# Kernel optimization log

Measured on AMD Instinct MI355X. Metric: run time of the kernel, lower is better.

The kernel has to match this reference:

```python
import jax, jax.numpy as jnp
import numpy as np

B, T, IN = 32, 1024, 256
H = 128          # hidden_size
NL = 2           # num_layers
NC = 4           # num_classes
F2 = 2 * H       # bidirectional feature size


def _lstm_dir(xs, w_ih, w_hh, b_ih, b_hh, reverse):
    # xs: [T, B, in]; w_ih: [4H, in]; w_hh: [4H, H]
    if reverse:
        xs = xs[::-1]
    h0 = jnp.zeros((xs.shape[1], H), xs.dtype)
    c0 = jnp.zeros((xs.shape[1], H), xs.dtype)

    def step(carry, xt):
        h, c = carry
        g = xt @ w_ih.T + b_ih + h @ w_hh.T + b_hh  # [B, 4H]
        i, f, gg, o = jnp.split(g, 4, axis=-1)       # PyTorch gate order i,f,g,o
        c = jax.nn.sigmoid(f) * c + jax.nn.sigmoid(i) * jnp.tanh(gg)
        h = jax.nn.sigmoid(o) * jnp.tanh(c)
        return (h, c), h

    _, hs = jax.lax.scan(step, (h0, c0), xs)  # [T, B, H]
    if reverse:
        hs = hs[::-1]
    return hs


def setup_inputs() -> dict:
    key = jax.random.key(0)
    ks = jax.random.split(key, 12)
    s = 0.05
    x = jax.random.normal(ks[0], (B, T, IN), jnp.float32)
    # stacked LSTM params: [layer, direction, ...]; layer0 in = IN, layer1 in = 2H = IN
    w_ih = jax.random.normal(ks[1], (NL, 2, 4 * H, IN), jnp.float32) * s
    w_hh = jax.random.normal(ks[2], (NL, 2, 4 * H, H), jnp.float32) * s
    b_ih = jax.random.normal(ks[3], (NL, 2, 4 * H), jnp.float32) * s
    b_hh = jax.random.normal(ks[4], (NL, 2, 4 * H), jnp.float32) * s
    wq = jax.random.normal(ks[5], (F2, F2), jnp.float32) * s
    wk = jax.random.normal(ks[6], (F2, F2), jnp.float32) * s
    wv = jax.random.normal(ks[7], (F2, F2), jnp.float32) * s
    bq = jax.random.normal(ks[8], (F2,), jnp.float32) * s
    bk = jax.random.normal(ks[9], (F2,), jnp.float32) * s
    bv = jax.random.normal(ks[10], (F2,), jnp.float32) * s
    w_fc = jax.random.normal(ks[11], (NC, F2), jnp.float32) * s
    b_fc = jnp.zeros((NC,), jnp.float32)
    return {"x": x, "w_ih": w_ih, "w_hh": w_hh, "b_ih": b_ih, "b_hh": b_hh,
            "wq": wq, "wk": wk, "wv": wv, "bq": bq, "bk": bk, "bv": bv,
            "w_fc": w_fc, "b_fc": b_fc}


def reference(x, w_ih, w_hh, b_ih, b_hh, wq, wk, wv, bq, bk, bv, w_fc, b_fc):
    # --- biLSTM (eval mode: inter-layer dropout inactive) ---
    xs = jnp.swapaxes(x, 0, 1)  # time-major [T, B, IN]
    for l in range(NL):
        fwd = _lstm_dir(xs, w_ih[l, 0], w_hh[l, 0], b_ih[l, 0], b_hh[l, 0], False)
        bwd = _lstm_dir(xs, w_ih[l, 1], w_hh[l, 1], b_ih[l, 1], b_hh[l, 1], True)
        xs = jnp.concatenate([fwd, bwd], axis=-1)  # [T, B, 2H]
    out = jnp.swapaxes(xs, 0, 1)  # [B, T, 2H]
    # --- naive full self-attention ---
    q = out @ wq.T + bq
    k = out @ wk.T + bk
    v = out @ wv.T + bv
    scores = jnp.einsum('btd,bsd->bts', q, k) / jnp.sqrt(jnp.float32(F2))
    attn = jax.nn.softmax(scores, axis=-1)          # [B, T, T]
    ctx = jnp.einsum('bts,bsd->btd', attn, v)       # [B, T, 2H]
    # --- FC head on last timestep ---
    return ctx[:, -1, :] @ w_fc.T + b_fc            # [B, NC]
```

## Files before the change

### kernel.cpp

```cpp
#include <hip/hip_runtime.h>
#include <math.h>
#include <stdint.h>

#define BB 32
#define TT 1024
#define INF 256
#define HH 128
#define G4 512
#define CH 16

typedef _Float16 half2_t __attribute__((ext_vector_type(2)));
typedef __attribute__((address_space(3))) uint32_t lds_u32;
typedef __attribute__((address_space(1))) const uint32_t glb_u32;

__device__ __forceinline__ float fdot2f(half2_t a, half2_t b, float c) {
    return __builtin_amdgcn_fdot2(a, b, c, false);
}
__device__ __forceinline__ float rcpf(float x) {
    return __builtin_amdgcn_rcpf(x);
}
__device__ __forceinline__ float dpp_xor1(float x) {
    return __builtin_bit_cast(float, __builtin_amdgcn_update_dpp(
        0, __builtin_bit_cast(int, x), 0xB1, 0xF, 0xF, true));
}
__device__ __forceinline__ float dpp_xor2(float x) {
    return __builtin_bit_cast(float, __builtin_amdgcn_update_dpp(
        0, __builtin_bit_cast(int, x), 0x4E, 0xF, 0xF, true));
}
__device__ __forceinline__ void bar_lgkm() {
    asm volatile("s_waitcnt lgkmcnt(0)\n\ts_barrier" ::: "memory");
}

__global__ __launch_bounds__(256, 2) void gemm_inproj(
    const float* __restrict__ A,
    const float* __restrict__ w_ih_l,
    const float* __restrict__ b_ih_l,
    const float* __restrict__ b_hh_l,
    float* __restrict__ xproj)
{
    const int d  = blockIdx.z;
    const float* W = w_ih_l + (size_t)d * G4 * INF;
    float* C = xproj + (size_t)d * 32768 * 512;
    const int m0 = blockIdx.y * 128;
    const int n0 = blockIdx.x * 128;
    const int tid = threadIdx.x;
    const int tx = tid & 15, ty = tid >> 4;

    __shared__ __align__(16) half2_t As2[16 * 128];
    __shared__ __align__(16) half2_t Bs2[16 * 128];

    float acc[8][8] = {};
    const int lr = tid >> 1;
    const int lk = (tid & 1) * 16;

    float4 ar4[4], br4[4];
#pragma unroll
    for (int i = 0; i < 4; ++i) {
        ar4[i] = *(const float4*)(A + (size_t)(m0 + lr) * 256 + lk + 4 * i);
        br4[i] = *(const float4*)(W + (size_t)(n0 + lr) * 256 + lk + 4 * i);
    }

    for (int k0 = 0; k0 < 256; k0 += 32) {
        __syncthreads();
#pragma unroll
        for (int i = 0; i < 4; ++i) {
            const int kp = (lk >> 1) + 2 * i;
            As2[(kp + 0) * 128 + lr] = half2_t{(_Float16)ar4[i].x, (_Float16)ar4[i].y};
            As2[(kp + 1) * 128 + lr] = half2_t{(_Float16)ar4[i].z, (_Float16)ar4[i].w};
            Bs2[(kp + 0) * 128 + lr] = half2_t{(_Float16)br4[i].x, (_Float16)br4[i].y};
            Bs2[(kp + 1) * 128 + lr] = half2_t{(_Float16)br4[i].z, (_Float16)br4[i].w};
        }
        __syncthreads();
        if (k0 + 32 < 256) {
#pragma unroll
            for (int i = 0; i < 4; ++i) {
                ar4[i] = *(const float4*)(A + (size_t)(m0 + lr) * 256 + k0 + 32 + lk + 4 * i);
                br4[i] = *(const float4*)(W + (size_t)(n0 + lr) * 256 + k0 + 32 + lk + 4 * i);
            }
        }
#pragma unroll
        for (int kp = 0; kp < 16; ++kp) {
            half2_t av[8], bv[8];
            *(float4*)&av[0] = *(const float4*)&As2[kp * 128 + ty * 4];
            *(float4*)&av[4] = *(const float4*)&As2[kp * 128 + 64 + ty * 4];
            *(float4*)&bv[0] = *(const float4*)&Bs2[kp * 128 + tx * 4];
            *(float4*)&bv[4] = *(const float4*)&Bs2[kp * 128 + 64 + tx * 4];
#pragma unroll
            for (int i = 0; i < 8; ++i)
#pragma unroll
                for (int j = 0; j < 8; ++j)
                    acc[i][j] = fdot2f(av[i], bv[j], acc[i][j]);
        }
    }

    float bias[8];
#pragma unroll
    for (int j = 0; j < 8; ++j) {
        const int n = n0 + (j < 4 ? tx * 4 + j : 64 + tx * 4 + (j - 4));
        bias[j] = b_ih_l[d * G4 + n] + b_hh_l[d * G4 + n];
    }
#pragma unroll
    for (int i = 0; i < 8; ++i) {
        const int m = m0 + (i < 4 ? ty * 4 + i : 64 + ty * 4 + (i - 4));
        float4 o0, o1;
        o0.x = acc[i][0] + bias[0]; o0.y = acc[i][1] + bias[1];
        o0.z = acc[i][2] + bias[2]; o0.w = acc[i][3] + bias[3];
        o1.x = acc[i][4] + bias[4]; o1.y = acc[i][5] + bias[5];
        o1.z = acc[i][6] + bias[6]; o1.w = acc[i][7] + bias[7];
        *(float4*)(C + (size_t)m * 512 + n0 + tx * 4)      = o0;
        *(float4*)(C + (size_t)m * 512 + n0 + 64 + tx * 4) = o1;
    }
}

__global__ __launch_bounds__(512, 1) void lstm_rec(
    const float* __restrict__ xproj,
    const float* __restrict__ w_hh_l,
    float* __restrict__ out)
{
    const int b = blockIdx.x & 31;
    const int d = blockIdx.x >> 5;
    const int tid = threadIdx.x;
    const int wvid = tid >> 6;
    const int l = tid & 63;
    const int s = l & 3;
    const int g = l >> 2;
    const int j = (wvid << 4) | g;

    __shared__ __align__(16) _Float16 hs[HH];
    __shared__ __align__(16) float xbuf[2][CH * 512];
    __shared__ __align__(16) float obuf[CH * HH];

    half2_t wv[4][16];
#pragma unroll
    for (int G = 0; G < 4; ++G) {
        const float* wr = w_hh_l + (size_t)(d * G4 + 128 * G + j) * HH + 32 * s;
#pragma unroll
        for (int q4 = 0; q4 < 8; ++q4) {
            float4 f = *(const float4*)(wr + 4 * q4);
            wv[G][2 * q4]     = half2_t{(_Float16)f.x, (_Float16)f.y};
            wv[G][2 * q4 + 1] = half2_t{(_Float16)f.z, (_Float16)f.w};
        }
    }

    if (tid < 64) ((half2_t*)hs)[tid] = half2_t{(_Float16)0.f, (_Float16)0.f};
    float c = 0.f;

    const float* xp = xproj + ((size_t)d * BB + b) * TT * 512;
    float* ob = out + (size_t)b * TT * 256 + d * HH;

    {
        const int tlo = d ? 1008 : 0;
        const float* gsrc = xp + (size_t)tlo * 512;
#pragma unroll
        for (int i = 0; i < 4; ++i)
            __builtin_amdgcn_global_load_lds((glb_u32*)(gsrc + tid * 4 + i * 2048),
                                             (lds_u32*)&xbuf[0][tid * 4 + i * 2048],
                                             16, 0, 0);
    }
    __syncthreads();

    for (int ck = 0; ck < 64; ++ck) {
        const int cur = ck & 1;
        if (ck + 1 < 64) {
            const int tlo = d ? (1008 - (ck + 1) * CH) : (ck + 1) * CH;
            const float* gsrc = xp + (size_t)tlo * 512;
#pragma unroll
            for (int i = 0; i < 4; ++i)
                __builtin_amdgcn_global_load_lds((glb_u32*)(gsrc + tid * 4 + i * 2048),
                                                 (lds_u32*)&xbuf[cur ^ 1][tid * 4 + i * 2048],
                                                 16, 0, 0);
        }
        const float* xb = xbuf[cur];

#pragma unroll 1
        for (int si = 0; si < CH; ++si) {
            const int lds_t = d ? (CH - 1 - si) : si;

            const float xi = xb[lds_t * 512 +       j];
            const float xf = xb[lds_t * 512 + 128 + j];
            const float xg = xb[lds_t * 512 + 256 + j];
            const float xo = xb[lds_t * 512 + 384 + j];

            const float4* hp = (const float4*)(hs + 32 * s);
            float4 hA = hp[0], hB = hp[1], hC = hp[2], hD = hp[3];
            half2_t hh[16];
            hh[0]  = __builtin_bit_cast(half2_t, hA.x);
            hh[1]  = __builtin_bit_cast(half2_t, hA.y);
            hh[2]  = __builtin_bit_cast(half2_t, hA.z);
            hh[3]  = __builtin_bit_cast(half2_t, hA.w);
            hh[4]  = __builtin_bit_cast(half2_t, hB.x);
            hh[5]  = __builtin_bit_cast(half2_t, hB.y);
            hh[6]  = __builtin_bit_cast(half2_t, hB.z);
            hh[7]  = __builtin_bit_cast(half2_t, hB.w);
            hh[8]  = __builtin_bit_cast(half2_t, hC.x);
            hh[9]  = __builtin_bit_cast(half2_t, hC.y);
            hh[10] = __builtin_bit_cast(half2_t, hC.z);
            hh[11] = __builtin_bit_cast(half2_t, hC.w);
            hh[12] = __builtin_bit_cast(half2_t, hD.x);
            hh[13] = __builtin_bit_cast(half2_t, hD.y);
            hh[14] = __builtin_bit_cast(half2_t, hD.z);
            hh[15] = __builtin_bit_cast(half2_t, hD.w);

            float a0 = 0.f, a1 = 0.f, a2 = 0.f, a3 = 0.f;
            float e0 = 0.f, e1 = 0.f, e2 = 0.f, e3 = 0.f;
#pragma unroll
            for (int kk = 0; kk < 8; ++kk) {
                a0 = fdot2f(wv[0][kk], hh[kk], a0);
                a1 = fdot2f(wv[1][kk], hh[kk], a1);
                a2 = fdot2f(wv[2][kk], hh[kk], a2);
                a3 = fdot2f(wv[3][kk], hh[kk], a3);
                e0 = fdot2f(wv[0][kk + 8], hh[kk + 8], e0);
                e1 = fdot2f(wv[1][kk + 8], hh[kk + 8], e1);
                e2 = fdot2f(wv[2][kk + 8], hh[kk + 8], e2);
                e3 = fdot2f(wv[3][kk + 8], hh[kk + 8], e3);
            }
            a0 += e0; a1 += e1; a2 += e2; a3 += e3;

            a0 += dpp_xor1(a0); a0 += dpp_xor2(a0);
            a1 += dpp_xor1(a1); a1 += dpp_xor2(a1);
            a2 += dpp_xor1(a2); a2 += dpp_xor2(a2);
            a3 += dpp_xor1(a3); a3 += dpp_xor2(a3);

            const float gi = rcpf(1.f + __expf(-(a0 + xi)));
            const float gf = rcpf(1.f + __expf(-(a1 + xf)));
            const float gg = 1.f - 2.f * rcpf(1.f + __expf(2.f * (a2 + xg)));
            const float go = rcpf(1.f + __expf(-(a3 + xo)));
            c = gf * c + gi * gg;
            const float th = 1.f - 2.f * rcpf(1.f + __expf(2.f * c));
            const float h = go * th;
            if (s == 0) {
                hs[j] = (_Float16)h;
                obuf[si * HH + j] = h;
            }
            bar_lgkm();
        }

        {
            const int idx = tid * 4;
            const int sf = idx >> 7, jf = idx & 127;
            const int sg = ck * CH + sf;
            const int t  = d ? (TT - 1 - sg) : sg;
            float4 o0 = *(const float4*)&obuf[idx];
            *(float4*)&ob[(size_t)t * 256 + jf] = o0;
        }
        __syncthreads();
    }
}

__global__ __launch_bounds__(256) void attn_kernel(
    const float* __restrict__ out1,
    const float* __restrict__ wq, const float* __restrict__ bq,
    const float* __restrict__ wk,
    const float* __restrict__ wv, const float* __restrict__ bv,
    const float* __restrict__ wfc, const float* __restrict__ bfc,
    float* __restrict__ outp)
{
    const int b = blockIdx.x;
    const int tid = threadIdx.x;
    __shared__ float xl[256], q[256], u[256], cx[256];
    __shared__ __align__(16) float r[256];
    __shared__ float sc[TT];
    __shared__ float red[256];

    const float* ob = out1 + (size_t)b * TT * 256;

    xl[tid] = ob[(size_t)(TT - 1) * 256 + tid];
    __syncthreads();

    float acc = bq[tid];
    const float* wqr = wq + (size_t)tid * 256;
#pragma unroll 4
    for (int k = 0; k < 256; ++k) acc += xl[k] * wqr[k];
    q[tid] = acc;
    __syncthreads();

    acc = 0.f;
#pragma unroll 4
    for (int dd = 0; dd < 256; ++dd) acc += q[dd] * wk[(size_t)dd * 256 + tid];
    r[tid] = acc;
    __syncthreads();

    const int wave = tid >> 6, lane = tid & 63;
    float4 r4 = *(const float4*)&r[lane * 4];
    for (int t = wave; t < TT; t += 4) {
        float4 o4 = *(const float4*)(ob + (size_t)t * 256 + lane * 4);
        float p = r4.x * o4.x + r4.y * o4.y + r4.z * o4.z + r4.w * o4.w;
#pragma unroll
        for (int off = 32; off > 0; off >>= 1) p += __shfl_down(p, off, 64);
        if (lane == 0) sc[t] = p * 0.0625f;
    }
    __syncthreads();

    float mx = -1e30f;
#pragma unroll
    for (int i = 0; i < 4; ++i) mx = fmaxf(mx, sc[tid + 256 * i]);
    red[tid] = mx; __syncthreads();
    for (int st = 128; st > 0; st >>= 1) {
        if (tid < st) red[tid] = fmaxf(red[tid], red[tid + st]);
        __syncthreads();
    }
    mx = red[0]; __syncthreads();
    float lsum = 0.f;
#pragma unroll
    for (int i = 0; i < 4; ++i) {
        float e = expf(sc[tid + 256 * i] - mx);
        sc[tid + 256 * i] = e;
        lsum += e;
    }
    __syncthreads();
    red[tid] = lsum; __syncthreads();
    for (int st = 128; st > 0; st >>= 1) {
        if (tid < st) red[tid] += red[tid + st];
        __syncthreads();
    }
    const float inv = 1.f / red[0];
    __syncthreads();

    acc = 0.f;
#pragma unroll 8
    for (int t = 0; t < TT; ++t) acc += sc[t] * ob[(size_t)t * 256 + tid];
    u[tid] = acc * inv;
    __syncthreads();

    acc = bv[tid];
#pragma unroll 4
    for (int k = 0; k < 256; ++k) acc += u[k] * wv[(size_t)tid * 256 + k];
    cx[tid] = acc;
    __syncthreads();

    if (tid < 4) {
        float o = bfc[tid];
        for (int k = 0; k < 256; ++k) o += cx[k] * wfc[tid * 256 + k];
        outp[b * 4 + tid] = o;
    }
}

extern "C" void kernel_launch(void* const* d_in, const int* in_sizes, int n_in,
                              void* d_out, int out_size, void* d_ws, size_t ws_size,
                              hipStream_t stream)
{
    const float* x    = (const float*)d_in[0];
    const float* w_ih = (const float*)d_in[1];
    const float* w_hh = (const float*)d_in[2];
    const float* b_ih = (const float*)d_in[3];
    const float* b_hh = (const float*)d_in[4];
    const float* wq   = (const float*)d_in[5];
    const float* wk   = (const float*)d_in[6];
    const float* wv   = (const float*)d_in[7];
    const float* bq   = (const float*)d_in[8];
    const float* bv   = (const float*)d_in[10];
    const float* wfc  = (const float*)d_in[11];
    const float* bfcv = (const float*)d_in[12];
    float* outp = (float*)d_out;

    float* ws    = (float*)d_ws;
    float* xproj = ws;
    float* out0  = ws + 33554432;
    float* out1  = out0 + 8388608;

    dim3 gg(4, 256, 2);

    gemm_inproj<<<gg, 256, 0, stream>>>(x, w_ih, b_ih, b_hh, xproj);
    lstm_rec<<<64, 512, 0, stream>>>(xproj, w_hh, out0);
    gemm_inproj<<<gg, 256, 0, stream>>>(out0, w_ih + 2 * 512 * 256, b_ih + 1024, b_hh + 1024, xproj);
    lstm_rec<<<64, 512, 0, stream>>>(xproj, w_hh + 2 * 512 * 128, out1);
    attn_kernel<<<32, 256, 0, stream>>>(out1, wq, bq, wk, wv, bv, wfc, bfcv, outp);
}
```

Measured before the change: 1.786 ms.

## Fuse input projection GEMM into LSTM recurrence kernel with chunk-ahead pipelining

Removes the separate input-projection GEMM and its large xproj buffer. Each LSTM block now computes the projection for the next time chunk itself, interleaved with the current chunk's serial recurrent steps, and reads fp16 W_ih converted once by a small kernel. This saves a large global write and read and two kernel launches. In exchange, the latency-bound recurrent loop gains extra per-step dot-product work and global weight loads, and only 64 blocks do the projection, so it may slow the serial critical path.

```diff
diff --git a/kernel.cpp b/kernel.cpp
--- a/kernel.cpp
+++ b/kernel.cpp
@@ -4,14 +4,11 @@
 
 #define BB 32
 #define TT 1024
-#define INF 256
 #define HH 128
 #define G4 512
 #define CH 16
 
 typedef _Float16 half2_t __attribute__((ext_vector_type(2)));
-typedef __attribute__((address_space(3))) uint32_t lds_u32;
-typedef __attribute__((address_space(1))) const uint32_t glb_u32;
 
 __device__ __forceinline__ float fdot2f(half2_t a, half2_t b, float c) {
     return __builtin_amdgcn_fdot2(a, b, c, false);
@@ -31,89 +28,21 @@
     asm volatile("s_waitcnt lgkmcnt(0)\n\ts_barrier" ::: "memory");
 }
 
-__global__ __launch_bounds__(256, 2) void gemm_inproj(
-    const float* __restrict__ A,
-    const float* __restrict__ w_ih_l,
+__global__ __launch_bounds__(256) void cvt_wih(
+    const float* __restrict__ w, _Float16* __restrict__ o)
+{
+    const int i = (blockIdx.x * 256 + threadIdx.x) * 4;
+    float4 f = *(const float4*)(w + i);
+    half2_t t[2] = { half2_t{(_Float16)f.x, (_Float16)f.y},
+                     half2_t{(_Float16)f.z, (_Float16)f.w} };
+    *(float2*)(o + i) = *(float2*)t;
+}
+
+__global__ __launch_bounds__(512, 1) void lstm_fused(
+    const float* __restrict__ x_in,
+    const _Float16* __restrict__ wih16_l,
     const float* __restrict__ b_ih_l,
     const float* __restrict__ b_hh_l,
-    float* __restrict__ xproj)
-{
-    const int d  = blockIdx.z;
-    const float* W = w_ih_l + (size_t)d * G4 * INF;
-    float* C = xproj + (size_t)d * 32768 * 512;
-    const int m0 = blockIdx.y * 128;
-    const int n0 = blockIdx.x * 128;
-    const int tid = threadIdx.x;
-    const int tx = tid & 15, ty = tid >> 4;
-
-    __shared__ __align__(16) half2_t As2[16 * 128];
-    __shared__ __align__(16) half2_t Bs2[16 * 128];
-
-    float acc[8][8] = {};
-    const int lr = tid >> 1;
-    const int lk = (tid & 1) * 16;
-
-    float4 ar4[4], br4[4];
-#pragma unroll
-    for (int i = 0; i < 4; ++i) {
-        ar4[i] = *(const float4*)(A + (size_t)(m0 + lr) * 256 + lk + 4 * i);
-        br4[i] = *(const float4*)(W + (size_t)(n0 + lr) * 256 + lk + 4 * i);
-    }
-
-    for (int k0 = 0; k0 < 256; k0 += 32) {
-        __syncthreads();
-#pragma unroll
-        for (int i = 0; i < 4; ++i) {
-            const int kp = (lk >> 1) + 2 * i;
-            As2[(kp + 0) * 128 + lr] = half2_t{(_Float16)ar4[i].x, (_Float16)ar4[i].y};
-            As2[(kp + 1) * 128 + lr] = half2_t{(_Float16)ar4[i].z, (_Float16)ar4[i].w};
-            Bs2[(kp + 0) * 128 + lr] = half2_t{(_Float16)br4[i].x, (_Float16)br4[i].y};
-            Bs2[(kp + 1) * 128 + lr] = half2_t{(_Float16)br4[i].z, (_Float16)br4[i].w};
-        }
-        __syncthreads();
-        if (k0 + 32 < 256) {
-#pragma unroll
-            for (int i = 0; i < 4; ++i) {
-                ar4[i] = *(const float4*)(A + (size_t)(m0 + lr) * 256 + k0 + 32 + lk + 4 * i);
-                br4[i] = *(const float4*)(W + (size_t)(n0 + lr) * 256 + k0 + 32 + lk + 4 * i);
-            }
-        }
-#pragma unroll
-        for (int kp = 0; kp < 16; ++kp) {
-            half2_t av[8], bv[8];
-            *(float4*)&av[0] = *(const float4*)&As2[kp * 128 + ty * 4];
-            *(float4*)&av[4] = *(const float4*)&As2[kp * 128 + 64 + ty * 4];
-            *(float4*)&bv[0] = *(const float4*)&Bs2[kp * 128 + tx * 4];
-            *(float4*)&bv[4] = *(const float4*)&Bs2[kp * 128 + 64 + tx * 4];
-#pragma unroll
-            for (int i = 0; i < 8; ++i)
-#pragma unroll
-                for (int j = 0; j < 8; ++j)
-                    acc[i][j] = fdot2f(av[i], bv[j], acc[i][j]);
-        }
-    }
-
-    float bias[8];
-#pragma unroll
-    for (int j = 0; j < 8; ++j) {
-        const int n = n0 + (j < 4 ? tx * 4 + j : 64 + tx * 4 + (j - 4));
-        bias[j] = b_ih_l[d * G4 + n] + b_hh_l[d * G4 + n];
-    }
-#pragma unroll
-    for (int i = 0; i < 8; ++i) {
-        const int m = m0 + (i < 4 ? ty * 4 + i : 64 + ty * 4 + (i - 4));
-        float4 o0, o1;
-        o0.x = acc[i][0] + bias[0]; o0.y = acc[i][1] + bias[1];
-        o0.z = acc[i][2] + bias[2]; o0.w = acc[i][3] + bias[3];
-        o1.x = acc[i][4] + bias[4]; o1.y = acc[i][5] + bias[5];
-        o1.z = acc[i][6] + bias[6]; o1.w = acc[i][7] + bias[7];
-        *(float4*)(C + (size_t)m * 512 + n0 + tx * 4)      = o0;
-        *(float4*)(C + (size_t)m * 512 + n0 + 64 + tx * 4) = o1;
-    }
-}
-
-__global__ __launch_bounds__(512, 1) void lstm_rec(
-    const float* __restrict__ xproj,
     const float* __restrict__ w_hh_l,
     float* __restrict__ out)
 {
@@ -127,7 +56,8 @@
     const int j = (wvid << 4) | g;
 
     __shared__ __align__(16) _Float16 hs[HH];
-    __shared__ __align__(16) float xbuf[2][CH * 512];
+    __shared__ __align__(16) float xp[2][CH * 512];
+    __shared__ __align__(16) half2_t xr[2][CH * 128];
     __shared__ __align__(16) float obuf[CH * HH];
 
     half2_t wv[4][16];
@@ -142,38 +72,67 @@
         }
     }
 
+    const _Float16* wrow = wih16_l + ((size_t)(d * G4 + tid)) * 256;
+    const float bias = b_ih_l[d * G4 + tid] + b_hh_l[d * G4 + tid];
+    const float* xbase = x_in + (size_t)b * TT * 256;
+
+#pragma unroll 1
+    for (int p = 0; p < 2; ++p) {
+        const int tlo = d ? (1008 - p * CH) : p * CH;
+        const float* gs = xbase + (size_t)tlo * 256 + tid * 8;
+        float4 f0 = *(const float4*)gs;
+        float4 f1 = *(const float4*)(gs + 4);
+        half2_t t4[4] = { half2_t{(_Float16)f0.x, (_Float16)f0.y},
+                          half2_t{(_Float16)f0.z, (_Float16)f0.w},
+                          half2_t{(_Float16)f1.x, (_Float16)f1.y},
+                          half2_t{(_Float16)f1.z, (_Float16)f1.w} };
+        *(float4*)&xr[p][tid * 4] = *(float4*)t4;
+    }
+    __syncthreads();
+
+    float acc[16];
+#pragma unroll
+    for (int sj = 0; sj < 16; ++sj) acc[sj] = bias;
+#pragma unroll 1
+    for (int kg = 0; kg < 16; ++kg) {
+        half2_t wk[8];
+        *(float4*)&wk[0] = *(const float4*)(wrow + kg * 16);
+        *(float4*)&wk[4] = *(const float4*)(wrow + kg * 16 + 8);
+#pragma unroll
+        for (int sj = 0; sj < 16; ++sj) {
+            half2_t xk[8];
+            *(float4*)&xk[0] = *(const float4*)&xr[0][sj * 128 + kg * 8];
+            *(float4*)&xk[4] = *(const float4*)&xr[0][sj * 128 + kg * 8 + 4];
+#pragma unroll
+            for (int kk = 0; kk < 8; ++kk) acc[sj] = fdot2f(wk[kk], xk[kk], acc[sj]);
+        }
+    }
+#pragma unroll
+    for (int sj = 0; sj < 16; ++sj) { xp[0][sj * 512 + tid] = acc[sj]; acc[sj] = bias; }
+
     if (tid < 64) ((half2_t*)hs)[tid] = half2_t{(_Float16)0.f, (_Float16)0.f};
     float c = 0.f;
-
-    const float* xp = xproj + ((size_t)d * BB + b) * TT * 512;
     float* ob = out + (size_t)b * TT * 256 + d * HH;
-
-    {
-        const int tlo = d ? 1008 : 0;
-        const float* gsrc = xp + (size_t)tlo * 512;
-#pragma unroll
-        for (int i = 0; i < 4; ++i)
-            __builtin_amdgcn_global_load_lds((glb_u32*)(gsrc + tid * 4 + i * 2048),
-                                             (lds_u32*)&xbuf[0][tid * 4 + i * 2048],
-                                             16, 0, 0);
-    }
-    __syncthreads();
-
+    __syncthreads();
+
+    float4 rg0 = {}, rg1 = {};
     for (int ck = 0; ck < 64; ++ck) {
         const int cur = ck & 1;
-        if (ck + 1 < 64) {
-            const int tlo = d ? (1008 - (ck + 1) * CH) : (ck + 1) * CH;
-            const float* gsrc = xp + (size_t)tlo * 512;
-#pragma unroll
-            for (int i = 0; i < 4; ++i)
-                __builtin_amdgcn_global_load_lds((glb_u32*)(gsrc + tid * 4 + i * 2048),
-                                                 (lds_u32*)&xbuf[cur ^ 1][tid * 4 + i * 2048],
-                                                 16, 0, 0);
-        }
-        const float* xb = xbuf[cur];
+        if (ck + 2 < 64) {
+            const int tlo2 = d ? (1008 - (ck + 2) * CH) : (ck + 2) * CH;
+            const float* gs = xbase + (size_t)tlo2 * 256 + tid * 8;
+            rg0 = *(const float4*)gs;
+            rg1 = *(const float4*)(gs + 4);
+        }
+        const float* xb = xp[cur];
+        const half2_t* xr_rd = xr[cur ^ 1];
 
 #pragma unroll 1
         for (int si = 0; si < CH; ++si) {
+            half2_t wk[8];
+            *(float4*)&wk[0] = *(const float4*)(wrow + si * 16);
+            *(float4*)&wk[4] = *(const float4*)(wrow + si * 16 + 8);
+
             const int lds_t = d ? (CH - 1 - si) : si;
 
             const float xi = xb[lds_t * 512 +       j];
@@ -232,6 +191,17 @@
                 hs[j] = (_Float16)h;
                 obuf[si * HH + j] = h;
             }
+
+#pragma unroll
+            for (int sj = 0; sj < 16; ++sj) {
+                half2_t xk[8];
+                *(float4*)&xk[0] = *(const float4*)&xr_rd[sj * 128 + si * 8];
+                *(float4*)&xk[4] = *(const float4*)&xr_rd[sj * 128 + si * 8 + 4];
+#pragma unroll
+                for (int kk = 0; kk < 8; ++kk)
+                    acc[sj] = fdot2f(wk[kk], xk[kk], acc[sj]);
+            }
+
             bar_lgkm();
         }
 
@@ -242,6 +212,18 @@
             const int t  = d ? (TT - 1 - sg) : sg;
             float4 o0 = *(const float4*)&obuf[idx];
             *(float4*)&ob[(size_t)t * 256 + jf] = o0;
+        }
+        {
+            float* xpn = xp[cur ^ 1];
+#pragma unroll
+            for (int sj = 0; sj < 16; ++sj) { xpn[sj * 512 + tid] = acc[sj]; acc[sj] = bias; }
+        }
+        if (ck + 2 < 64) {
+            half2_t t4[4] = { half2_t{(_Float16)rg0.x, (_Float16)rg0.y},
+                              half2_t{(_Float16)rg0.z, (_Float16)rg0.w},
+                              half2_t{(_Float16)rg1.x, (_Float16)rg1.y},
+                              half2_t{(_Float16)rg1.z, (_Float16)rg1.w} };
+            *(float4*)&xr[cur][tid * 4] = *(float4*)t4;
         }
         __syncthreads();
     }
@@ -353,16 +335,15 @@
     const float* bfcv = (const float*)d_in[12];
     float* outp = (float*)d_out;
 
-    float* ws    = (float*)d_ws;
-    float* xproj = ws;
-    float* out0  = ws + 33554432;
-    float* out1  = out0 + 8388608;
-
-    dim3 gg(4, 256, 2);
-
-    gemm_inproj<<<gg, 256, 0, stream>>>(x, w_ih, b_ih, b_hh, xproj);
-    lstm_rec<<<64, 512, 0, stream>>>(xproj, w_hh, out0);
-    gemm_inproj<<<gg, 256, 0, stream>>>(out0, w_ih + 2 * 512 * 256, b_ih + 1024, b_hh + 1024, xproj);
-    lstm_rec<<<64, 512, 0, stream>>>(xproj, w_hh + 2 * 512 * 128, out1);
+    float* ws = (float*)d_ws;
+    _Float16* wih16 = (_Float16*)ws;
+    float* out0 = ws + 262144;
+    float* out1 = out0 + 8388608;
+
+    cvt_wih<<<512, 256, 0, stream>>>(w_ih, wih16);
+
+    lstm_fused<<<64, 512, 0, stream>>>(x, wih16, b_ih, b_hh, w_hh, out0);
+    lstm_fused<<<64, 512, 0, stream>>>(out0, wih16 + 262144, b_ih + 1024, b_hh + 1024,
+                                       w_hh + 2 * 512 * 128, out1);
     attn_kernel<<<32, 256, 0, stream>>>(out1, wq, bq, wk, wv, bv, wfc, bfcv, outp);
 }
```

After: 3.269 ms. 1.83x slower.
